# Performance work log

Hardware: AMD Instinct MI355X
Metric: run time of the kernel (lower is better)

## Reference

```python
import jax, jax.numpy as jnp
import numpy as np

N_COL, N_ROW = 256, 256  # grid_size = (n_col, n_row); n_row = grid_size[1], n_col = grid_size[0]
N_AGENTS, N_POINTS = 64, 1001  # agent_len=1000 -> 1001 samples per trajectory
BATCH = 512


def setup_inputs() -> dict:
    key = jax.random.key(0)
    k1, k2, k3 = jax.random.split(key, 3)
    inp = jax.random.normal(k1, (BATCH, N_COL * N_ROW), dtype=jnp.float32)
    agents_x = jax.random.uniform(k2, (N_AGENTS, N_POINTS), dtype=jnp.float32)
    agents_y = jax.random.uniform(k3, (N_AGENTS, N_POINTS), dtype=jnp.float32)
    return {"input": inp, "agents_x": agents_x, "agents_y": agents_y}


def _touch_mask(agents_x, agents_y):
    # Cell (i,j) box: [i/n_col + 1/(4*n_col), i/n_col + 3/(4*n_col)] x (same in y).
    # Equivalently: frac = p*n - floor(p*n) must lie in [0.25, 0.75] on both axes,
    # and the point then touches exactly the cell it falls inside of.
    fx = agents_x * N_COL
    fy = agents_y * N_ROW
    cx = jnp.floor(fx)
    cy = jnp.floor(fy)
    rx = fx - cx
    ry = fy - cy
    in_box = (rx >= 0.25) & (rx <= 0.75) & (ry >= 0.25) & (ry <= 0.75)
    ix = jnp.clip(cx.astype(jnp.int32), 0, N_COL - 1)
    iy = jnp.clip(cy.astype(jnp.int32), 0, N_ROW - 1)
    flat = (ix * N_ROW + iy).reshape(-1)
    touched = jnp.zeros(N_COL * N_ROW, dtype=jnp.int32).at[flat].max(
        in_box.reshape(-1).astype(jnp.int32)
    )
    # is_touching[i,j] = 1 unless some agent point is in the box -> 0
    mask = 1.0 - touched.astype(jnp.float32)  # [n_col*n_row]
    mask = jnp.rot90(mask.reshape(N_COL, N_ROW))  # torch.rot90 default: CCW, dims (0,1)
    return mask.reshape(-1)


def reference(input, agents_x, agents_y):
    mask = _touch_mask(agents_x, agents_y)  # [n_neurons]
    n_neurons = N_COL * N_ROW
    dropout_rate = 1.0 - jnp.sum(mask) / n_neurons
    return input * mask * (1.0 / (1.0 - dropout_rate))
```

## Files before the change

kernel.cpp:

```cpp
#include <hip/hip_runtime.h>

#define N_COL 256
#define N_ROW 256
#define N_NEUR (N_COL * N_ROW)
#define N_PTS  (64 * 1001)
#define BATCH  512

__global__ void scatter_touch(const float* __restrict__ ax,
                              const float* __restrict__ ay,
                              int* __restrict__ touched) {
    int p = blockIdx.x * blockDim.x + threadIdx.x;
    if (p >= N_PTS) return;
    float fx = ax[p] * (float)N_COL;
    float fy = ay[p] * (float)N_ROW;
    float cx = floorf(fx);
    float cy = floorf(fy);
    float rx = fx - cx;
    float ry = fy - cy;
    bool in_box = (rx >= 0.25f) && (rx <= 0.75f) && (ry >= 0.25f) && (ry <= 0.75f);
    if (in_box) {
        int ix = min(max((int)cx, 0), N_COL - 1);
        int iy = min(max((int)cy, 0), N_ROW - 1);
        touched[ix * N_ROW + iy] = 1;
    }
}

__global__ void build_mask(const int* __restrict__ touched,
                           float* __restrict__ mask_rot,
                           int* __restrict__ sum_out) {
    int k = blockIdx.x * blockDim.x + threadIdx.x;
    int i = k >> 8;
    int j = k & 255;
    int src = j * N_ROW + (N_ROW - 1 - i);
    int m = 1 - touched[src];
    mask_rot[k] = (float)m;
    unsigned long long b = __ballot(m != 0);
    if ((threadIdx.x & 63) == 0) {
        atomicAdd(sum_out, (int)__popcll(b));
    }
}

__global__ void apply_mask(const float* __restrict__ in,
                           const float* __restrict__ mask_rot,
                           const int* __restrict__ sum_ptr,
                           float* __restrict__ out) {
    const unsigned total4 = (unsigned)BATCH * (N_NEUR / 4);
    float s = (float)(*sum_ptr);
    float rate = 1.0f - s / (float)N_NEUR;
    float scale = 1.0f / (1.0f - rate);

    const float4* __restrict__ in4   = (const float4*)in;
    const float4* __restrict__ mask4 = (const float4*)mask_rot;
    float4* __restrict__ out4        = (float4*)out;

    unsigned stride = gridDim.x * blockDim.x;
    for (unsigned idx = blockIdx.x * blockDim.x + threadIdx.x;
         idx < total4; idx += stride) {
        unsigned mIdx = idx & (N_NEUR / 4 - 1);
        float4 v = in4[idx];
        float4 m = mask4[mIdx];
        float4 r;
        r.x = v.x * m.x * scale;
        r.y = v.y * m.y * scale;
        r.z = v.z * m.z * scale;
        r.w = v.w * m.w * scale;
        out4[idx] = r;
    }
}

extern "C" void kernel_launch(void* const* d_in, const int* in_sizes, int n_in,
                              void* d_out, int out_size, void* d_ws, size_t ws_size,
                              hipStream_t stream) {
    const float* input = (const float*)d_in[0];
    const float* ax    = (const float*)d_in[1];
    const float* ay    = (const float*)d_in[2];
    float* out = (float*)d_out;

    int*   touched  = (int*)d_ws;
    int*   sum_out  = touched + N_NEUR;
    float* mask_rot = (float*)((char*)d_ws + (N_NEUR + 4) * sizeof(int));

    hipMemsetAsync(touched, 0, (N_NEUR + 1) * sizeof(int), stream);

    scatter_touch<<<(N_PTS + 255) / 256, 256, 0, stream>>>(ax, ay, touched);
    build_mask<<<N_NEUR / 256, 256, 0, stream>>>(touched, mask_rot, sum_out);
    apply_mask<<<2048, 256, 0, stream>>>(input, mask_rot, sum_out, out);
}
```

Measured before the change: 253.8 us.

## Scatter directly into rotated float mask and use nontemporal loads/stores

Drops the separate touched buffer and build_mask pass. A small init kernel fills the rotated float mask with 1.0, and the scatter kernel atomically zeroes the rotated cell while counting first-time clears to get the kept-neuron sum. The apply kernel now uses nontemporal loads and stores on the streaming input and output so they do not pollute cache. Overall time is dominated by the 128MB streaming pass, so the launch and pass savings are small relative to it.

```diff
diff --git a/kernel.cpp b/kernel.cpp
--- a/kernel.cpp
+++ b/kernel.cpp
@@ -6,9 +6,19 @@
 #define N_PTS  (64 * 1001)
 #define BATCH  512
 
+typedef float f32x4 __attribute__((ext_vector_type(4)));
+
+
+__global__ void init_mask(float* __restrict__ mask, int* __restrict__ count) {
+    int k = blockIdx.x * blockDim.x + threadIdx.x;
+    mask[k] = 1.0f;
+    if (k == 0) *count = 0;
+}
+
 __global__ void scatter_touch(const float* __restrict__ ax,
                               const float* __restrict__ ay,
-                              int* __restrict__ touched) {
+                              int* __restrict__ mask_bits,
+                              int* __restrict__ count) {
     int p = blockIdx.x * blockDim.x + threadIdx.x;
     if (p >= N_PTS) return;
     float fx = ax[p] * (float)N_COL;
@@ -21,50 +31,33 @@
     if (in_box) {
         int ix = min(max((int)cx, 0), N_COL - 1);
         int iy = min(max((int)cy, 0), N_ROW - 1);
-        touched[ix * N_ROW + iy] = 1;
-    }
-}
-
-__global__ void build_mask(const int* __restrict__ touched,
-                           float* __restrict__ mask_rot,
-                           int* __restrict__ sum_out) {
-    int k = blockIdx.x * blockDim.x + threadIdx.x;
-    int i = k >> 8;
-    int j = k & 255;
-    int src = j * N_ROW + (N_ROW - 1 - i);
-    int m = 1 - touched[src];
-    mask_rot[k] = (float)m;
-    unsigned long long b = __ballot(m != 0);
-    if ((threadIdx.x & 63) == 0) {
-        atomicAdd(sum_out, (int)__popcll(b));
+        int k = (N_ROW - 1 - iy) * N_COL + ix;
+        int old = atomicExch(&mask_bits[k], 0);
+        if (old != 0) atomicAdd(count, 1);
     }
 }
 
 __global__ void apply_mask(const float* __restrict__ in,
                            const float* __restrict__ mask_rot,
-                           const int* __restrict__ sum_ptr,
+                           const int* __restrict__ count_ptr,
                            float* __restrict__ out) {
     const unsigned total4 = (unsigned)BATCH * (N_NEUR / 4);
-    float s = (float)(*sum_ptr);
+    float s = (float)(N_NEUR - *count_ptr);
     float rate = 1.0f - s / (float)N_NEUR;
     float scale = 1.0f / (1.0f - rate);
 
-    const float4* __restrict__ in4   = (const float4*)in;
-    const float4* __restrict__ mask4 = (const float4*)mask_rot;
-    float4* __restrict__ out4        = (float4*)out;
+    const f32x4* __restrict__ in4   = (const f32x4*)in;
+    const f32x4* __restrict__ mask4 = (const f32x4*)mask_rot;
+    f32x4* __restrict__ out4        = (f32x4*)out;
 
     unsigned stride = gridDim.x * blockDim.x;
     for (unsigned idx = blockIdx.x * blockDim.x + threadIdx.x;
          idx < total4; idx += stride) {
         unsigned mIdx = idx & (N_NEUR / 4 - 1);
-        float4 v = in4[idx];
-        float4 m = mask4[mIdx];
-        float4 r;
-        r.x = v.x * m.x * scale;
-        r.y = v.y * m.y * scale;
-        r.z = v.z * m.z * scale;
-        r.w = v.w * m.w * scale;
-        out4[idx] = r;
+        f32x4 v = __builtin_nontemporal_load(&in4[idx]);
+        f32x4 m = mask4[mIdx];
+        f32x4 r = v * m * scale;
+        __builtin_nontemporal_store(r, &out4[idx]);
     }
 }
 
@@ -76,13 +69,11 @@
     const float* ay    = (const float*)d_in[2];
     float* out = (float*)d_out;
 
-    int*   touched  = (int*)d_ws;
-    int*   sum_out  = touched + N_NEUR;
-    float* mask_rot = (float*)((char*)d_ws + (N_NEUR + 4) * sizeof(int));
+    float* mask_rot = (float*)d_ws;
+    int*   count    = (int*)d_ws + N_NEUR;
 
-    hipMemsetAsync(touched, 0, (N_NEUR + 1) * sizeof(int), stream);
-
-    scatter_touch<<<(N_PTS + 255) / 256, 256, 0, stream>>>(ax, ay, touched);
-    build_mask<<<N_NEUR / 256, 256, 0, stream>>>(touched, mask_rot, sum_out);
-    apply_mask<<<2048, 256, 0, stream>>>(input, mask_rot, sum_out, out);
+    init_mask<<<N_NEUR / 256, 256, 0, stream>>>(mask_rot, count);
+    scatter_touch<<<(N_PTS + 255) / 256, 256, 0, stream>>>(
+        ax, ay, (int*)mask_rot, count);
+    apply_mask<<<2048, 256, 0, stream>>>(input, mask_rot, count, out);
 }
```

After: 240.0 us. 5.4% less time.
